# Kernel tuning notes

Measured on AMD Instinct MI355X. Metric: run time of the kernel, lower is better.

## Reference

```python
import jax, jax.numpy as jnp
import numpy as np

# dims
N, E, HID = 20000, 320000, 128
L, H = 12, 4            # num_layers, heads
C = 2 * HID             # h width = in_channels = out_channels*heads = 256
OC = C // H             # per-head out channels = 64
FF = 4 * HID            # ffn hidden = 512
LN_EPS = 1e-5
SLOPE = 0.2             # GATConv leaky_relu negative slope


def _layer_norm(x, g, b):
    m = x.mean(-1, keepdims=True)
    v = ((x - m) ** 2).mean(-1, keepdims=True)
    return (x - m) * jax.lax.rsqrt(v + LN_EPS) * g + b


def setup_inputs() -> dict:
    key = jax.random.key(0)
    ks = jax.random.split(key, 16)
    s = 0.05
    f32 = jnp.float32
    return {
        "hf": jax.random.normal(ks[0], (N, HID), f32),
        "hs": jax.random.normal(ks[1], (N, HID), f32),
        "edge_index": jax.random.randint(ks[2], (2, E), 0, N, dtype=jnp.int32),
        # GATConv params (stacked over layers)
        "W": jax.random.normal(ks[3], (L, C, H * OC), f32) * s,       # lin (no bias)
        "att_src": jax.random.normal(ks[4], (L, H, OC), f32) * s,
        "att_dst": jax.random.normal(ks[5], (L, H, OC), f32) * s,
        "gat_b": jax.random.normal(ks[6], (L, C), f32) * s,            # GATConv bias
        # FFN params
        "w1": jax.random.normal(ks[7], (L, C, FF), f32) * s,
        "b1": jax.random.normal(ks[8], (L, FF), f32) * s,
        "w2": jax.random.normal(ks[9], (L, FF, C), f32) * s,
        "b2": jax.random.normal(ks[10], (L, C), f32) * s,
        # LayerNorm params
        "ln1_g": jnp.ones((L, C), f32),
        "ln1_b": jnp.zeros((L, C), f32),
        "ln2_g": jnp.ones((L, C), f32),
        "ln2_b": jnp.zeros((L, C), f32),
    }


def reference(hf, hs, edge_index, W, att_src, att_dst, gat_b,
              w1, b1, w2, b2, ln1_g, ln1_b, ln2_g, ln2_b):
    # PyG GATConv add_self_loops=True
    loop = jnp.arange(N, dtype=edge_index.dtype)
    src = jnp.concatenate([edge_index[0], loop])  # [E+N]
    dst = jnp.concatenate([edge_index[1], loop])

    h = jnp.concatenate([hf, hs], axis=-1)  # [N, C]
    for i in range(L):
        # --- GATConv + residual + LN (dropout = identity at eval) ---
        r = h
        xh = (h @ W[i]).reshape(N, H, OC)              # [N,H,OC]
        a_s = (xh * att_src[i]).sum(-1)                # [N,H]
        a_d = (xh * att_dst[i]).sum(-1)                # [N,H]
        e = jax.nn.leaky_relu(a_s[src] + a_d[dst], SLOPE)          # [E+N,H]
        m = jax.ops.segment_max(e, dst, num_segments=N)            # [N,H]
        ex = jnp.exp(e - m[dst])
        z = jax.ops.segment_sum(ex, dst, num_segments=N)           # [N,H]
        alpha = ex / z[dst]                                        # segment softmax
        msg = xh[src] * alpha[..., None]                           # [E+N,H,OC]
        out = jax.ops.segment_sum(msg, dst, num_segments=N).reshape(N, C) + gat_b[i]
        h = _layer_norm(out + r, ln1_g[i], ln1_b[i])
        # --- FFN + residual + LN ---
        r = h
        f = jax.nn.relu(h @ w1[i] + b1[i]) @ w2[i] + b2[i]
        h = _layer_norm(f + r, ln2_g[i], ln2_b[i])

    return h[:, :HID], h[:, HID:]
```

## Files before the change

### kernel.cpp

```cpp
#include <hip/hip_runtime.h>
#include <hip/hip_bf16.h>
#include <math.h>

#define C_DIM 256
#define HID 128
#define HEADS 4
#define OC 64
#define FF_DIM 512
#define NLAYERS 12

constexpr float LN_EPS = 1e-5f;
constexpr float SLOPE  = 0.2f;

typedef __attribute__((ext_vector_type(4))) float f32x4;
typedef __attribute__((ext_vector_type(8))) short bf16x8_t;
typedef __attribute__((ext_vector_type(4))) int i32x4;

__device__ __forceinline__ float leaky(float x) { return x > 0.f ? x : SLOPE * x; }

__device__ __forceinline__ float bf2f(unsigned short u) {
    union { unsigned i; float f; } v; v.i = ((unsigned)u) << 16; return v.f;
}
__device__ __forceinline__ void bf2x(unsigned u, float& lo, float& hi) {
    union { unsigned i; float f; } a, b;
    a.i = u << 16; b.i = u & 0xffff0000u;
    lo = a.f; hi = b.f;
}
__device__ __forceinline__ unsigned packbf(float lo, float hi) {
    unsigned a = __bfloat16_as_ushort(__float2bfloat16(lo));
    unsigned b = __bfloat16_as_ushort(__float2bfloat16(hi));
    return a | (b << 16);
}

__global__ void zero_i32_kernel(int* __restrict__ p, int n) {
    int i = blockIdx.x * blockDim.x + threadIdx.x;
    if (i < n) p[i] = 0;
}

__global__ void concat_kernel(const float* __restrict__ hf, const float* __restrict__ hs,
                              __hip_bfloat16* __restrict__ hb, int Nn) {
    int idx = blockIdx.x * blockDim.x + threadIdx.x;
    int total = Nn * C_DIM;
    if (idx < total) {
        int n = idx >> 8;
        int c = idx & 255;
        float v = (c < HID) ? hf[n * HID + c] : hs[n * HID + (c - HID)];
        hb[idx] = __float2bfloat16(v);
    }
}

__global__ void transp_bf16_kernel(const float* __restrict__ in,
                                   __hip_bfloat16* __restrict__ out, int K, int N) {
    __shared__ float t[32][33];
    const float* inl = in + (size_t)blockIdx.z * K * N;
    __hip_bfloat16* outl = out + (size_t)blockIdx.z * K * N;
    int kb = blockIdx.y * 32, nb = blockIdx.x * 32;
    int tx = threadIdx.x & 31, ty = threadIdx.x >> 5;
    #pragma unroll
    for (int r = 0; r < 32; r += 8)
        t[ty + r][tx] = inl[(size_t)(kb + ty + r) * N + nb + tx];
    __syncthreads();
    #pragma unroll
    for (int r = 0; r < 32; r += 8)
        outl[(size_t)(nb + ty + r) * K + kb + tx] = __float2bfloat16(t[tx][ty + r]);
}

__global__ void hist_kernel(const int* __restrict__ dst, int* __restrict__ counts, int E) {
    int e = blockIdx.x * blockDim.x + threadIdx.x;
    if (e < E) atomicAdd(&counts[dst[e]], 1);
}

__global__ void scan_kernel(const int* __restrict__ counts, int* __restrict__ offsets,
                            int* __restrict__ cursor, int n) {
    __shared__ int wsum[16];
    __shared__ int carry_s;
    const int lane = threadIdx.x & 63, wid = threadIdx.x >> 6;
    if (threadIdx.x == 0) carry_s = 0;
    __syncthreads();
    for (int base = 0; base < n; base += 1024) {
        int i = base + (int)threadIdx.x;
        int v = (i < n) ? counts[i] : 0;
        int x = v;
        #pragma unroll
        for (int off = 1; off < 64; off <<= 1) {
            int t = __shfl_up(x, off);
            if (lane >= off) x += t;
        }
        if (lane == 63) wsum[wid] = x;
        __syncthreads();
        if (threadIdx.x == 0) {
            int acc = carry_s;
            #pragma unroll
            for (int w = 0; w < 16; ++w) { int t = wsum[w]; wsum[w] = acc; acc += t; }
            carry_s = acc;
        }
        __syncthreads();
        int excl = wsum[wid] + x - v;
        if (i < n) { offsets[i] = excl; cursor[i] = excl; }
        __syncthreads();
    }
    if (threadIdx.x == 0) offsets[n] = carry_s;
}

__global__ void fill_kernel(const int* __restrict__ src, const int* __restrict__ dst,
                            int* __restrict__ cursor, int* __restrict__ csr_src, int E) {
    int e = blockIdx.x * blockDim.x + threadIdx.x;
    if (e < E) {
        int d = dst[e];
        int p = atomicAdd(&cursor[d], 1);
        csr_src[p] = src[e];
    }
}

#define GBM 64
#define GBN 128
#define GBK 64
#define GLS 72

__global__ __launch_bounds__(256) void gemm_bf16_kernel(
    const __hip_bfloat16* __restrict__ A,
    const __hip_bfloat16* __restrict__ BT,
    const float* __restrict__ bias,
    __hip_bfloat16* __restrict__ Cb,
    const float* __restrict__ attS,
    const float* __restrict__ attD,
    float* __restrict__ aS,
    float* __restrict__ aD,
    int M, int N, int K, int relu)
{
    __shared__ short As[GBM * GLS];
    __shared__ short Bs[GBN * GLS];
    const int tid = threadIdx.x;
    const int wave = tid >> 6, lane = tid & 63;
    const int lr = lane & 15, lq = lane >> 4;
    const int wm = (wave >> 1) * 32, wn = (wave & 1) * 64;
    const int row0 = blockIdx.x * GBM, col0 = blockIdx.y * GBN;

    const int sra = tid >> 2;
    const int sca = (tid & 3) * 16;
    const int srb = tid >> 1;
    const int scb = (tid & 1) * 32;

    f32x4 acc[2][4] = {};

    for (int k0 = 0; k0 < K; k0 += GBK) {
        const __hip_bfloat16* ap = &A[(size_t)(row0 + sra) * K + k0 + sca];
        i32x4 va0 = *(const i32x4*)ap;
        i32x4 va1 = *(const i32x4*)(ap + 8);
        const __hip_bfloat16* bp = &BT[(size_t)(col0 + srb) * K + k0 + scb];
        i32x4 vb0 = *(const i32x4*)bp;
        i32x4 vb1 = *(const i32x4*)(bp + 8);
        i32x4 vb2 = *(const i32x4*)(bp + 16);
        i32x4 vb3 = *(const i32x4*)(bp + 24);
        *(i32x4*)&As[sra * GLS + sca] = va0;
        *(i32x4*)&As[sra * GLS + sca + 8] = va1;
        *(i32x4*)&Bs[srb * GLS + scb] = vb0;
        *(i32x4*)&Bs[srb * GLS + scb + 8] = vb1;
        *(i32x4*)&Bs[srb * GLS + scb + 16] = vb2;
        *(i32x4*)&Bs[srb * GLS + scb + 24] = vb3;
        __syncthreads();

        #pragma unroll
        for (int ks = 0; ks < 2; ++ks) {
            bf16x8_t af[2], bfr[4];
            #pragma unroll
            for (int t = 0; t < 2; ++t)
                af[t]  = *(const bf16x8_t*)&As[(wm + t * 16 + lr) * GLS + ks * 32 + lq * 8];
            #pragma unroll
            for (int t = 0; t < 4; ++t)
                bfr[t] = *(const bf16x8_t*)&Bs[(wn + t * 16 + lr) * GLS + ks * 32 + lq * 8];
            #pragma unroll
            for (int mt = 0; mt < 2; ++mt)
                #pragma unroll
                for (int nt = 0; nt < 4; ++nt)
                    acc[mt][nt] = __builtin_amdgcn_mfma_f32_16x16x32_bf16(
                        af[mt], bfr[nt], acc[mt][nt], 0, 0, 0);
        }
        __syncthreads();
    }

    float bv[4];
    #pragma unroll
    for (int nt = 0; nt < 4; ++nt)
        bv[nt] = bias ? bias[col0 + wn + nt * 16 + lr] : 0.f;

    #pragma unroll
    for (int mt = 0; mt < 2; ++mt) {
        #pragma unroll
        for (int r = 0; r < 4; ++r) {
            int grow = row0 + wm + mt * 16 + lq * 4 + r;
            if (grow >= M) continue;
            #pragma unroll
            for (int nt = 0; nt < 4; ++nt) {
                float v = acc[mt][nt][r] + bv[nt];
                if (relu) v = fmaxf(v, 0.f);
                Cb[(size_t)grow * N + col0 + wn + nt * 16 + lr] = __float2bfloat16(v);
            }
        }
    }

    if (aS) {
        const int head = (col0 + wn) >> 6;
        float atS[4], atD[4];
        #pragma unroll
        for (int nt = 0; nt < 4; ++nt) {
            int c = col0 + wn + nt * 16 + lr;
            atS[nt] = attS[c];
            atD[nt] = attD[c];
        }
        #pragma unroll
        for (int mt = 0; mt < 2; ++mt) {
            #pragma unroll
            for (int r = 0; r < 4; ++r) {
                float vs = acc[mt][0][r] * atS[0] + acc[mt][1][r] * atS[1]
                         + acc[mt][2][r] * atS[2] + acc[mt][3][r] * atS[3];
                float vd = acc[mt][0][r] * atD[0] + acc[mt][1][r] * atD[1]
                         + acc[mt][2][r] * atD[2] + acc[mt][3][r] * atD[3];
                #pragma unroll
                for (int off = 1; off < 16; off <<= 1) {
                    vs += __shfl_xor(vs, off);
                    vd += __shfl_xor(vd, off);
                }
                if (lr == 0) {
                    int grow = row0 + wm + mt * 16 + lq * 4 + r;
                    if (grow < M) {
                        aS[grow * HEADS + head] = vs;
                        aD[grow * HEADS + head] = vd;
                    }
                }
            }
        }
    }
}

#define FBM 32

__global__ __launch_bounds__(256) void gemm3_ln_kernel(
    const __hip_bfloat16* __restrict__ A,
    const __hip_bfloat16* __restrict__ BT,
    const float* __restrict__ bias,
    const float* __restrict__ ln_g, const float* __restrict__ ln_b,
    __hip_bfloat16* __restrict__ hb,
    float* __restrict__ out_split,
    int M)
{
    __shared__ short As[FBM * GLS];
    __shared__ short Bs[C_DIM * GLS];
    __shared__ float rsum[2][FBM][4];

    const int tid = threadIdx.x;
    const int wave = tid >> 6, lane = tid & 63;
    const int lr = lane & 15, lq = lane >> 4;
    const int wn = wave * 64;
    const int row0 = blockIdx.x * FBM;

    const int sr = tid >> 2;
    const int sc = (tid & 3) * 16;

    f32x4 acc[2][4] = {};

    for (int k0 = 0; k0 < FF_DIM; k0 += GBK) {
        if (sr < FBM) {
            const __hip_bfloat16* ap = &A[(size_t)(row0 + sr) * FF_DIM + k0 + sc];
            *(i32x4*)&As[sr * GLS + sc] = *(const i32x4*)ap;
            *(i32x4*)&As[sr * GLS + sc + 8] = *(const i32x4*)(ap + 8);
        }
        #pragma unroll
        for (int rb = 0; rb < 4; ++rb) {
            const int br = rb * 64 + sr;
            const __hip_bfloat16* bp = &BT[(size_t)br * FF_DIM + k0 + sc];
            *(i32x4*)&Bs[br * GLS + sc] = *(const i32x4*)bp;
            *(i32x4*)&Bs[br * GLS + sc + 8] = *(const i32x4*)(bp + 8);
        }
        __syncthreads();

        #pragma unroll
        for (int ks = 0; ks < 2; ++ks) {
            bf16x8_t af[2], bfr[4];
            #pragma unroll
            for (int mt = 0; mt < 2; ++mt)
                af[mt] = *(const bf16x8_t*)&As[(mt * 16 + lr) * GLS + ks * 32 + lq * 8];
            #pragma unroll
            for (int nt = 0; nt < 4; ++nt)
                bfr[nt] = *(const bf16x8_t*)&Bs[(wn + nt * 16 + lr) * GLS + ks * 32 + lq * 8];
            #pragma unroll
            for (int mt = 0; mt < 2; ++mt)
                #pragma unroll
                for (int nt = 0; nt < 4; ++nt)
                    acc[mt][nt] = __builtin_amdgcn_mfma_f32_16x16x32_bf16(
                        af[mt], bfr[nt], acc[mt][nt], 0, 0, 0);
        }
        __syncthreads();
    }

    float bv[4];
    #pragma unroll
    for (int nt = 0; nt < 4; ++nt)
        bv[nt] = bias[wn + nt * 16 + lr];

    const unsigned short* hbp = (const unsigned short*)hb;
    #pragma unroll
    for (int mt = 0; mt < 2; ++mt) {
        #pragma unroll
        for (int r = 0; r < 4; ++r) {
            const int rb = mt * 16 + lq * 4 + r;
            const int grow = row0 + rb;
            float s1 = 0.f, s2 = 0.f;
            #pragma unroll
            for (int nt = 0; nt < 4; ++nt) {
                float res = (grow < M)
                    ? bf2f(hbp[(size_t)grow * C_DIM + wn + nt * 16 + lr]) : 0.f;
                float v = acc[mt][nt][r] + bv[nt] + res;
                acc[mt][nt][r] = v;
                s1 += v; s2 += v * v;
            }
            #pragma unroll
            for (int off = 1; off < 16; off <<= 1) {
                s1 += __shfl_xor(s1, off);
                s2 += __shfl_xor(s2, off);
            }
            if (lr == 0) {
                rsum[0][rb][wave] = s1;
                rsum[1][rb][wave] = s2;
            }
        }
    }
    __syncthreads();

    float g[4], bb[4];
    #pragma unroll
    for (int nt = 0; nt < 4; ++nt) {
        g[nt]  = ln_g[wn + nt * 16 + lr];
        bb[nt] = ln_b[wn + nt * 16 + lr];
    }

    #pragma unroll
    for (int mt = 0; mt < 2; ++mt) {
        #pragma unroll
        for (int r = 0; r < 4; ++r) {
            const int rb = mt * 16 + lq * 4 + r;
            const int grow = row0 + rb;
            if (grow >= M) continue;
            float s1 = (rsum[0][rb][0] + rsum[0][rb][1]) + (rsum[0][rb][2] + rsum[0][rb][3]);
            float s2 = (rsum[1][rb][0] + rsum[1][rb][1]) + (rsum[1][rb][2] + rsum[1][rb][3]);
            float mean = s1 * (1.0f / C_DIM);
            float inv = rsqrtf(s2 * (1.0f / C_DIM) - mean * mean + LN_EPS);
            if (out_split) {
                #pragma unroll
                for (int nt = 0; nt < 4; ++nt) {
                    float o = (acc[mt][nt][r] - mean) * inv * g[nt] + bb[nt];
                    int c = wn + nt * 16 + lr;
                    size_t off_ = (c < HID) ? ((size_t)grow * HID + c)
                                            : ((size_t)M * HID + (size_t)grow * HID + (c - HID));
                    out_split[off_] = o;
                }
            } else {
                #pragma unroll
                for (int nt = 0; nt < 4; ++nt) {
                    float o = (acc[mt][nt][r] - mean) * inv * g[nt] + bb[nt];
                    ((unsigned short*)hb)[(size_t)grow * C_DIM + wn + nt * 16 + lr] =
                        __bfloat16_as_ushort(__float2bfloat16(o));
                }
            }
        }
    }
}

__global__ __launch_bounds__(256) void agg_kernel(
    const __hip_bfloat16* __restrict__ xhb, const float* __restrict__ a_s,
    const float* __restrict__ a_d, const int* __restrict__ csr,
    const int* __restrict__ offs, const float* __restrict__ gat_b,
    const float* __restrict__ ln_g, const float* __restrict__ ln_b,
    __hip_bfloat16* __restrict__ hb, int Nn)
{
    const int lane = threadIdx.x & 63;
    const int n = __builtin_amdgcn_readfirstlane(blockIdx.x * 4 + (threadIdx.x >> 6));
    if (n >= Nn) return;
    const int half = lane >> 5;
    const int sl = lane & 31;
    const int head = sl >> 3;
    const int c0 = sl * 8;
    const unsigned* x = (const unsigned*)xhb;
    const size_t rowp = (size_t)n * (C_DIM / 2) + (c0 >> 1);

    const float ad = a_d[n * 4 + head];

    const int beg = offs[n], end = offs[n + 1];
    const int ne = end - beg;
    const int nh0 = (ne + 1) >> 1;
    int ih  = half ? (beg + nh0) : beg;
    int cnt = half ? (ne - nh0) : nh0;

    i32x4 rv = *(const i32x4*)&((const unsigned*)hb)[rowp];

    float acc[8] = {};
    float z = 0.f;

    {
        float wself = __expf(leaky(a_s[n * 4 + head] + ad));
        if (half) {
            i32x4 xv = *(const i32x4*)&x[rowp];
            #pragma unroll
            for (int q = 0; q < 4; ++q) {
                float lo, hi; bf2x((unsigned)xv[q], lo, hi);
                acc[2 * q]     = wself * lo;
                acc[2 * q + 1] = wself * hi;
            }
            z = wself;
        }
    }

    for (; cnt >= 4; cnt -= 4, ih += 4) {
        int s0 = csr[ih], s1 = csr[ih + 1], s2 = csr[ih + 2], s3 = csr[ih + 3];
        float w0 = __expf(leaky(a_s[s0 * 4 + head] + ad));
        float w1 = __expf(leaky(a_s[s1 * 4 + head] + ad));
        float w2 = __expf(leaky(a_s[s2 * 4 + head] + ad));
        float w3 = __expf(leaky(a_s[s3 * 4 + head] + ad));
        i32x4 x0 = *(const i32x4*)&x[(size_t)s0 * (C_DIM / 2) + (c0 >> 1)];
        i32x4 x1 = *(const i32x4*)&x[(size_t)s1 * (C_DIM / 2) + (c0 >> 1)];
        i32x4 x2 = *(const i32x4*)&x[(size_t)s2 * (C_DIM / 2) + (c0 >> 1)];
        i32x4 x3 = *(const i32x4*)&x[(size_t)s3 * (C_DIM / 2) + (c0 >> 1)];
        #pragma unroll
        for (int q = 0; q < 4; ++q) {
            float lo, hi;
            bf2x((unsigned)x0[q], lo, hi);
            acc[2 * q] += w0 * lo; acc[2 * q + 1] += w0 * hi;
            bf2x((unsigned)x1[q], lo, hi);
            acc[2 * q] += w1 * lo; acc[2 * q + 1] += w1 * hi;
            bf2x((unsigned)x2[q], lo, hi);
            acc[2 * q] += w2 * lo; acc[2 * q + 1] += w2 * hi;
            bf2x((unsigned)x3[q], lo, hi);
            acc[2 * q] += w3 * lo; acc[2 * q + 1] += w3 * hi;
        }
        z += (w0 + w1) + (w2 + w3);
    }
    for (; cnt > 0; --cnt, ++ih) {
        int s0 = csr[ih];
        float w0 = __expf(leaky(a_s[s0 * 4 + head] + ad));
        i32x4 x0 = *(const i32x4*)&x[(size_t)s0 * (C_DIM / 2) + (c0 >> 1)];
        #pragma unroll
        for (int q = 0; q < 4; ++q) {
            float lo, hi; bf2x((unsigned)x0[q], lo, hi);
            acc[2 * q] += w0 * lo; acc[2 * q + 1] += w0 * hi;
        }
        z += w0;
    }

    #pragma unroll
    for (int j = 0; j < 8; ++j) acc[j] += __shfl_xor(acc[j], 32);
    z += __shfl_xor(z, 32);

    float res[8];
    #pragma unroll
    for (int q = 0; q < 4; ++q) bf2x((unsigned)rv[q], res[2 * q], res[2 * q + 1]);

    float4 gb0 = *(const float4*)&gat_b[c0];
    float4 gb1 = *(const float4*)&gat_b[c0 + 4];
    float gb[8] = {gb0.x, gb0.y, gb0.z, gb0.w, gb1.x, gb1.y, gb1.z, gb1.w};
    float rz = 1.0f / z;
    float val[8];
    #pragma unroll
    for (int j = 0; j < 8; ++j) val[j] = acc[j] * rz + gb[j] + res[j];

    float s1 = 0.f, s2 = 0.f;
    #pragma unroll
    for (int j = 0; j < 8; ++j) { s1 += val[j]; s2 += val[j] * val[j]; }
    #pragma unroll
    for (int off = 1; off < 64; off <<= 1) {
        s1 += __shfl_xor(s1, off);
        s2 += __shfl_xor(s2, off);
    }
    float mean = s1 * (1.0f / (2 * C_DIM));
    float inv = rsqrtf(s2 * (1.0f / (2 * C_DIM)) - mean * mean + LN_EPS);

    if (half == 0) {
        float4 g0 = *(const float4*)&ln_g[c0];
        float4 g1 = *(const float4*)&ln_g[c0 + 4];
        float4 bb0 = *(const float4*)&ln_b[c0];
        float4 bb1 = *(const float4*)&ln_b[c0 + 4];
        float g[8] = {g0.x, g0.y, g0.z, g0.w, g1.x, g1.y, g1.z, g1.w};
        float bb[8] = {bb0.x, bb0.y, bb0.z, bb0.w, bb1.x, bb1.y, bb1.z, bb1.w};
        float o[8];
        #pragma unroll
        for (int j = 0; j < 8; ++j) o[j] = (val[j] - mean) * inv * g[j] + bb[j];
        i32x4 ob;
        ob[0] = (int)packbf(o[0], o[1]);
        ob[1] = (int)packbf(o[2], o[3]);
        ob[2] = (int)packbf(o[4], o[5]);
        ob[3] = (int)packbf(o[6], o[7]);
        *(i32x4*)&((unsigned*)hb)[rowp] = ob;
    }
}

extern "C" void kernel_launch(void* const* d_in, const int* in_sizes, int n_in,
                              void* d_out, int out_size, void* d_ws, size_t ws_size,
                              hipStream_t stream)
{
    const float* hf       = (const float*)d_in[0];
    const float* hs       = (const float*)d_in[1];
    const int*   edge     = (const int*)  d_in[2];
    const float* W        = (const float*)d_in[3];
    const float* att_src  = (const float*)d_in[4];
    const float* att_dst  = (const float*)d_in[5];
    const float* gat_b    = (const float*)d_in[6];
    const float* w1       = (const float*)d_in[7];
    const float* b1       = (const float*)d_in[8];
    const float* w2       = (const float*)d_in[9];
    const float* b2       = (const float*)d_in[10];
    const float* ln1g     = (const float*)d_in[11];
    const float* ln1b     = (const float*)d_in[12];
    const float* ln2g     = (const float*)d_in[13];
    const float* ln2b     = (const float*)d_in[14];
    float* out = (float*)d_out;

    const int N = in_sizes[0] / HID;
    const int E = in_sizes[2] / 2;
    const int* e_src = edge;
    const int* e_dst = edge + E;

    char* p = (char*)d_ws;
    auto alloc = [&](size_t bytes) {
        char* r = p;
        p += (bytes + 255) & ~(size_t)255;
        return (void*)r;
    };
    const int NPAD = N + 64;
    __hip_bfloat16* hb     = (__hip_bfloat16*)alloc((size_t)NPAD * C_DIM * 2);
    __hip_bfloat16* xhb    = (__hip_bfloat16*)alloc((size_t)N * C_DIM * 2);
    __hip_bfloat16* midb   = (__hip_bfloat16*)alloc((size_t)N * FF_DIM * 2);
    float*          a_s    = (float*)alloc((size_t)N * HEADS * 4);
    float*          a_d    = (float*)alloc((size_t)N * HEADS * 4);
    int*            counts = (int*)alloc((size_t)N * 4);
    int*            offs   = (int*)alloc((size_t)(N + 1) * 4);
    int*            cursor = (int*)alloc((size_t)N * 4);
    int*            csr    = (int*)alloc((size_t)E * 4);
    __hip_bfloat16* WT     = (__hip_bfloat16*)alloc((size_t)NLAYERS * C_DIM * C_DIM * 2);
    __hip_bfloat16* w1T    = (__hip_bfloat16*)alloc((size_t)NLAYERS * C_DIM * FF_DIM * 2);
    __hip_bfloat16* w2T    = (__hip_bfloat16*)alloc((size_t)NLAYERS * FF_DIM * C_DIM * 2);

    {
        int total = N * C_DIM;
        concat_kernel<<<(total + 255) / 256, 256, 0, stream>>>(hf, hs, hb, N);
    }
    transp_bf16_kernel<<<dim3(C_DIM / 32, C_DIM / 32, NLAYERS), 256, 0, stream>>>(W, WT, C_DIM, C_DIM);
    transp_bf16_kernel<<<dim3(FF_DIM / 32, C_DIM / 32, NLAYERS), 256, 0, stream>>>(w1, w1T, C_DIM, FF_DIM);
    transp_bf16_kernel<<<dim3(C_DIM / 32, FF_DIM / 32, NLAYERS), 256, 0, stream>>>(w2, w2T, FF_DIM, C_DIM);

    zero_i32_kernel<<<(N + 255) / 256, 256, 0, stream>>>(counts, N);
    hist_kernel<<<(E + 255) / 256, 256, 0, stream>>>(e_dst, counts, E);
    scan_kernel<<<1, 1024, 0, stream>>>(counts, offs, cursor, N);
    fill_kernel<<<(E + 255) / 256, 256, 0, stream>>>(e_src, e_dst, cursor, csr, E);

    const int gm = (N + GBM - 1) / GBM;
    const int gf = (N + FBM - 1) / FBM;

    for (int l = 0; l < NLAYERS; ++l) {
        const __hip_bfloat16* Wl  = WT  + (size_t)l * C_DIM * C_DIM;
        const __hip_bfloat16* w1l = w1T + (size_t)l * C_DIM * FF_DIM;
        const __hip_bfloat16* w2l = w2T + (size_t)l * FF_DIM * C_DIM;
        const float* asl  = att_src + (size_t)l * C_DIM;
        const float* adl  = att_dst + (size_t)l * C_DIM;
        const float* gbl  = gat_b + (size_t)l * C_DIM;
        const float* b1l  = b1 + (size_t)l * FF_DIM;
        const float* b2l  = b2 + (size_t)l * C_DIM;
        const float* g1l  = ln1g + (size_t)l * C_DIM;
        const float* be1l = ln1b + (size_t)l * C_DIM;
        const float* g2l  = ln2g + (size_t)l * C_DIM;
        const float* be2l = ln2b + (size_t)l * C_DIM;

        gemm_bf16_kernel<<<dim3(gm, C_DIM / GBN), 256, 0, stream>>>(
            hb, Wl, nullptr, xhb, asl, adl, a_s, a_d, N, C_DIM, C_DIM, 0);
        agg_kernel<<<(N + 3) / 4, 256, 0, stream>>>(
            xhb, a_s, a_d, csr, offs, gbl, g1l, be1l, hb, N);
        gemm_bf16_kernel<<<dim3(gm, FF_DIM / GBN), 256, 0, stream>>>(
            hb, w1l, b1l, midb, nullptr, nullptr, nullptr, nullptr,
            N, FF_DIM, C_DIM, 1);
        gemm3_ln_kernel<<<gf, 256, 0, stream>>>(
            midb, w2l, b2l, g2l, be2l, hb,
            (l == NLAYERS - 1) ? out : nullptr, N);
    }
}
```

Measured before the change: 1.139 ms.

## Double row tile of FFN2+LN GEMM to 64 rows with 512-thread blocks

Raises the row tile of the second FFN GEMM with fused LayerNorm from 32 to 64 rows and uses 8 waves in a 2x4 grid instead of 4. Each 256-wide weight tile loaded into shared memory is now reused across twice as many rows, which cuts redundant B-tile traffic. Global loads are issued into registers before the shared-memory stores, and the intermediate buffer is padded so the unguarded A loads on the last block stay in bounds. In exchange, fewer blocks are launched and each block uses more shared memory.

```diff
diff --git a/kernel.cpp b/kernel.cpp
--- a/kernel.cpp
+++ b/kernel.cpp
@@ -233,9 +233,9 @@
     }
 }
 
-#define FBM 32
-
-__global__ __launch_bounds__(256) void gemm3_ln_kernel(
+#define FBM 64
+
+__global__ __launch_bounds__(512) void gemm3_ln_kernel(
     const __hip_bfloat16* __restrict__ A,
     const __hip_bfloat16* __restrict__ BT,
     const float* __restrict__ bias,
@@ -251,27 +251,26 @@
     const int tid = threadIdx.x;
     const int wave = tid >> 6, lane = tid & 63;
     const int lr = lane & 15, lq = lane >> 4;
-    const int wn = wave * 64;
+    const int wm = (wave >> 2) * 32;
+    const int wn = (wave & 3) * 64;
     const int row0 = blockIdx.x * FBM;
 
-    const int sr = tid >> 2;
-    const int sc = (tid & 3) * 16;
+    const int sr = tid >> 3;
+    const int sc = (tid & 7) * 8;
 
     f32x4 acc[2][4] = {};
 
     for (int k0 = 0; k0 < FF_DIM; k0 += GBK) {
-        if (sr < FBM) {
-            const __hip_bfloat16* ap = &A[(size_t)(row0 + sr) * FF_DIM + k0 + sc];
-            *(i32x4*)&As[sr * GLS + sc] = *(const i32x4*)ap;
-            *(i32x4*)&As[sr * GLS + sc + 8] = *(const i32x4*)(ap + 8);
-        }
-        #pragma unroll
-        for (int rb = 0; rb < 4; ++rb) {
-            const int br = rb * 64 + sr;
-            const __hip_bfloat16* bp = &BT[(size_t)br * FF_DIM + k0 + sc];
-            *(i32x4*)&Bs[br * GLS + sc] = *(const i32x4*)bp;
-            *(i32x4*)&Bs[br * GLS + sc + 8] = *(const i32x4*)(bp + 8);
-        }
+        const __hip_bfloat16* ap = &A[(size_t)(row0 + sr) * FF_DIM + k0 + sc];
+        i32x4 va = *(const i32x4*)ap;
+        i32x4 vb[4];
+        #pragma unroll
+        for (int rb = 0; rb < 4; ++rb)
+            vb[rb] = *(const i32x4*)&BT[(size_t)(rb * 64 + sr) * FF_DIM + k0 + sc];
+        *(i32x4*)&As[sr * GLS + sc] = va;
+        #pragma unroll
+        for (int rb = 0; rb < 4; ++rb)
+            *(i32x4*)&Bs[(rb * 64 + sr) * GLS + sc] = vb[rb];
         __syncthreads();
 
         #pragma unroll
@@ -279,7 +278,7 @@
             bf16x8_t af[2], bfr[4];
             #pragma unroll
             for (int mt = 0; mt < 2; ++mt)
-                af[mt] = *(const bf16x8_t*)&As[(mt * 16 + lr) * GLS + ks * 32 + lq * 8];
+                af[mt] = *(const bf16x8_t*)&As[(wm + mt * 16 + lr) * GLS + ks * 32 + lq * 8];
             #pragma unroll
             for (int nt = 0; nt < 4; ++nt)
                 bfr[nt] = *(const bf16x8_t*)&Bs[(wn + nt * 16 + lr) * GLS + ks * 32 + lq * 8];
@@ -303,7 +302,7 @@
     for (int mt = 0; mt < 2; ++mt) {
         #pragma unroll
         for (int r = 0; r < 4; ++r) {
-            const int rb = mt * 16 + lq * 4 + r;
+            const int rb = wm + mt * 16 + lq * 4 + r;
             const int grow = row0 + rb;
             float s1 = 0.f, s2 = 0.f;
             #pragma unroll
@@ -320,8 +319,8 @@
                 s2 += __shfl_xor(s2, off);
             }
             if (lr == 0) {
-                rsum[0][rb][wave] = s1;
-                rsum[1][rb][wave] = s2;
+                rsum[0][rb][wave & 3] = s1;
+                rsum[1][rb][wave & 3] = s2;
             }
         }
     }
@@ -338,7 +337,7 @@
     for (int mt = 0; mt < 2; ++mt) {
         #pragma unroll
         for (int r = 0; r < 4; ++r) {
-            const int rb = mt * 16 + lq * 4 + r;
+            const int rb = wm + mt * 16 + lq * 4 + r;
             const int grow = row0 + rb;
             if (grow >= M) continue;
             float s1 = (rsum[0][rb][0] + rsum[0][rb][1]) + (rsum[0][rb][2] + rsum[0][rb][3]);
@@ -527,7 +526,7 @@
     const int NPAD = N + 64;
     __hip_bfloat16* hb     = (__hip_bfloat16*)alloc((size_t)NPAD * C_DIM * 2);
     __hip_bfloat16* xhb    = (__hip_bfloat16*)alloc((size_t)N * C_DIM * 2);
-    __hip_bfloat16* midb   = (__hip_bfloat16*)alloc((size_t)N * FF_DIM * 2);
+    __hip_bfloat16* midb   = (__hip_bfloat16*)alloc((size_t)NPAD * FF_DIM * 2);
     float*          a_s    = (float*)alloc((size_t)N * HEADS * 4);
     float*          a_d    = (float*)alloc((size_t)N * HEADS * 4);
     int*            counts = (int*)alloc((size_t)N * 4);
@@ -575,7 +574,7 @@
         gemm_bf16_kernel<<<dim3(gm, FF_DIM / GBN), 256, 0, stream>>>(
             hb, w1l, b1l, midb, nullptr, nullptr, nullptr, nullptr,
             N, FF_DIM, C_DIM, 1);
-        gemm3_ln_kernel<<<gf, 256, 0, stream>>>(
+        gemm3_ln_kernel<<<gf, 512, 0, stream>>>(
             midb, w2l, b2l, g2l, be2l, hb,
             (l == NLAYERS - 1) ? out : nullptr, N);
     }
```

Measured after the change: 1.173 ms. +3.0%, slower.
